# Performance work log

Hardware: AMD Instinct MI355X
Metric: run time of the kernel (lower is better)

The kernel has to match this reference:

```python
import jax, jax.numpy as jnp
import numpy as np

N_NODES = 50000
N_EDGES = 800000
F_IN = 64
CHANNELS = 64
ATTN_SLOPE = 0.2   # GATConv internal LeakyReLU on attention logits
OUT_SLOPE = 0.3    # wrapper's LeakyReLU(alpha=0.3)


def setup_inputs() -> dict:
    key = jax.random.key(0)
    ks = jax.random.split(key, 7)
    x = jax.random.normal(ks[0], (N_NODES, F_IN), dtype=jnp.float32)
    edge_src = jax.random.randint(ks[1], (N_EDGES,), 0, N_NODES, dtype=jnp.int64)
    edge_dst = jax.random.randint(ks[2], (N_EDGES,), 0, N_NODES, dtype=jnp.int64)
    # Learned parameters (single attention head)
    W = jax.random.normal(ks[3], (F_IN, CHANNELS), dtype=jnp.float32) / np.sqrt(F_IN)
    a_src = jax.random.normal(ks[4], (CHANNELS,), dtype=jnp.float32) / np.sqrt(CHANNELS)
    a_dst = jax.random.normal(ks[5], (CHANNELS,), dtype=jnp.float32) / np.sqrt(CHANNELS)
    b = jnp.zeros((CHANNELS,), dtype=jnp.float32)
    return {"x": x, "W": W, "a_src": a_src, "a_dst": a_dst, "b": b,
            "edge_src": edge_src, "edge_dst": edge_dst}


def reference(x, W, a_src, a_dst, b, edge_src, edge_dst):
    N = x.shape[0]
    h = x @ W                                  # [N, C] transformed features
    s_src = h @ a_src                          # [N] per-node source score
    s_dst = h @ a_dst                          # [N] per-node dest score
    # Per-edge attention logits, LeakyReLU(0.2) as in GAT
    e = jax.nn.leaky_relu(s_src[edge_src] + s_dst[edge_dst], ATTN_SLOPE)  # [E]
    # Numerically stable softmax over each destination's neighborhood
    m = jax.ops.segment_max(e, edge_dst, num_segments=N)                  # [N]
    ex = jnp.exp(e - m[edge_dst])                                         # [E]
    denom = jax.ops.segment_sum(ex, edge_dst, num_segments=N)             # [N]
    alpha = ex / jnp.maximum(denom[edge_dst], 1e-9)                       # [E]
    # Scatter-aggregate weighted neighbor features
    out = jax.ops.segment_sum(alpha[:, None] * h[edge_src], edge_dst,
                              num_segments=N) + b                         # [N, C]
    return jax.nn.leaky_relu(out, OUT_SLOPE)
```

## Files before the change

kernel.cpp:

```cpp
#include <hip/hip_runtime.h>
#include <hip/hip_fp16.h>

#define N_NODES 50000
#define N_EDGES 800000
#define CH 64
#define FT_NODES 32
#define FT_BLKS ((N_NODES + FT_NODES - 1) / FT_NODES)
#define NB 782
#define NCHK 784
#define ECHUNK ((N_EDGES + NCHK - 1) / NCHK)
#define LCAP 2048

static constexpr size_t alignup16(size_t x) { return (x + 15) & ~(size_t)15; }
static const size_t OFF_H      = 0;
static const size_t OFF_SSRC   = alignup16(OFF_H      + (size_t)N_NODES*CH*2);
static const size_t OFF_SDST   = alignup16(OFF_SSRC   + (size_t)N_NODES*4);
static const size_t OFF_HIST   = alignup16(OFF_SDST   + (size_t)N_NODES*4);
static const size_t OFF_BTOT   = alignup16(OFF_HIST   + (size_t)NCHK*NB*4);
static const size_t OFF_CB     = alignup16(OFF_BTOT   + (size_t)NB*4);
static const size_t OFF_ROWPTR = alignup16(OFF_CB     + (size_t)(NB+1)*4);
static const size_t OFF_BUCK   = alignup16(OFF_ROWPTR + (size_t)(N_NODES+4)*4);
static const size_t OFF_SPERM  = alignup16(OFF_BUCK   + (size_t)N_EDGES*4);

__global__ __launch_bounds__(256) void k_feat(
        const float* __restrict__ x, const float* __restrict__ W,
        const float* __restrict__ a_src, const float* __restrict__ a_dst,
        const int* __restrict__ edst,
        __half* __restrict__ h, float* __restrict__ ssrc, float* __restrict__ sdst,
        unsigned int* __restrict__ hist) {
    __shared__ float Ws[64 * 64];
    __shared__ float xs[FT_NODES][68];
    __shared__ unsigned int lh[NB];
    const int tid = threadIdx.x;
    const bool do_hist = (blockIdx.x < NCHK);
    if (do_hist)
        for (int j = tid; j < NB; j += 256) lh[j] = 0u;
#pragma unroll
    for (int i = 0; i < 16; ++i) Ws[tid + i * 256] = W[tid + i * 256];
    const int n0 = blockIdx.x * FT_NODES;
    const int nvalid = min(FT_NODES, N_NODES - n0);
    const float4* x4 = (const float4*)(x + (size_t)n0 * CH);
    for (int i = tid; i < nvalid * 16; i += 256) {
        const int n = i >> 4, q = i & 15;
        *(float4*)&xs[n][q * 4] = x4[i];
    }
    __syncthreads();
    if (do_hist) {
        const int st = blockIdx.x * ECHUNK;
        const int en = min(st + ECHUNK, N_EDGES);
        for (int i = st + tid; i < en; i += 256)
            atomicAdd(&lh[((unsigned int)edst[i]) >> 6], 1u);
    }
    const int nl = tid >> 3;
    const int g = tid & 7;
    const int c0 = g * 8;
    const int node = n0 + nl;
    if (nl < nvalid) {
        float acc[8] = {0.f, 0.f, 0.f, 0.f, 0.f, 0.f, 0.f, 0.f};
#pragma unroll
        for (int k = 0; k < 64; ++k) {
            const float xv = xs[nl][k];
            const float4 w0 = *(const float4*)&Ws[k * 64 + c0];
            const float4 w1 = *(const float4*)&Ws[k * 64 + c0 + 4];
            acc[0] = fmaf(xv, w0.x, acc[0]);
            acc[1] = fmaf(xv, w0.y, acc[1]);
            acc[2] = fmaf(xv, w0.z, acc[2]);
            acc[3] = fmaf(xv, w0.w, acc[3]);
            acc[4] = fmaf(xv, w1.x, acc[4]);
            acc[5] = fmaf(xv, w1.y, acc[5]);
            acc[6] = fmaf(xv, w1.z, acc[6]);
            acc[7] = fmaf(xv, w1.w, acc[7]);
        }
        __half2 hv[4];
#pragma unroll
        for (int i = 0; i < 4; ++i) hv[i] = __floats2half2_rn(acc[2 * i], acc[2 * i + 1]);
        *(float4*)(h + (size_t)node * CH + c0) = *(float4*)hv;
        float ps = 0.f, pd = 0.f;
#pragma unroll
        for (int i = 0; i < 8; ++i) {
            ps = fmaf(acc[i], a_src[c0 + i], ps);
            pd = fmaf(acc[i], a_dst[c0 + i], pd);
        }
#pragma unroll
        for (int off = 4; off; off >>= 1) {
            ps += __shfl_xor(ps, off);
            pd += __shfl_xor(pd, off);
        }
        if (g == 0) { ssrc[node] = ps; sdst[node] = pd; }
    }
    if (do_hist) {
        __syncthreads();
        for (int j = tid; j < NB; j += 256)
            hist[(size_t)blockIdx.x * NB + j] = lh[j];
    }
}

__global__ __launch_bounds__(256) void k_bintot(
        const unsigned int* __restrict__ hist, unsigned int* __restrict__ bintot) {
    __shared__ unsigned int red[256];
    const int t = threadIdx.x, b = blockIdx.x;
    unsigned int v = 0u;
    for (int c = t; c < NCHK; c += 256) v += hist[(size_t)c * NB + b];
    red[t] = v;
    __syncthreads();
#pragma unroll
    for (int off = 128; off; off >>= 1) {
        if (t < off) red[t] += red[t + off];
        __syncthreads();
    }
    if (t == 0) bintot[b] = red[0];
}

__global__ __launch_bounds__(256) void k_rewrite(
        const unsigned int* __restrict__ bintot, unsigned int* __restrict__ hist,
        unsigned int* __restrict__ cb) {
    __shared__ unsigned int lcol[NCHK];
    __shared__ unsigned int red[256];
    __shared__ unsigned int sc[256];
    const int t = threadIdx.x, b = blockIdx.x;
    unsigned int v = 0u;
    for (int j = t; j < b; j += 256) v += bintot[j];
    red[t] = v;
    for (int c = t; c < NCHK; c += 256) lcol[c] = hist[(size_t)c * NB + b];
    __syncthreads();
#pragma unroll
    for (int off = 128; off; off >>= 1) {
        if (t < off) red[t] += red[t + off];
        __syncthreads();
    }
    const unsigned int cbb = red[0];
    if (t == 0) { cb[b] = cbb; if (b == NB - 1) cb[NB] = N_EDGES; }
    unsigned int part = 0u;
    const int c0 = 4 * t;
    if (t < 196) {
#pragma unroll
        for (int q = 0; q < 4; ++q) part += lcol[c0 + q];
    }
    sc[t] = part;
    __syncthreads();
#pragma unroll
    for (int off = 1; off < 256; off <<= 1) {
        unsigned int u = (t >= off) ? sc[t - off] : 0u;
        __syncthreads();
        sc[t] += u;
        __syncthreads();
    }
    if (t < 196) {
        unsigned int run = cbb + sc[t] - part;
#pragma unroll
        for (int q = 0; q < 4; ++q) {
            const unsigned int tmp = lcol[c0 + q];
            lcol[c0 + q] = run;
            run += tmp;
        }
    }
    __syncthreads();
    for (int c = t; c < NCHK; c += 256) hist[(size_t)c * NB + b] = lcol[c];
}

__global__ __launch_bounds__(256) void k_scatter(
        const int* __restrict__ esrc, const int* __restrict__ edst,
        const unsigned int* __restrict__ hist, unsigned int* __restrict__ buck) {
    __shared__ unsigned int wp[NB];
    const int t = threadIdx.x, blk = blockIdx.x;
    for (int j = t; j < NB; j += 256) wp[j] = hist[(size_t)blk * NB + j];
    __syncthreads();
    const int st = blk * ECHUNK;
    const int en = min(st + ECHUNK, N_EDGES);
    for (int i = st + t; i < en; i += 256) {
        const unsigned int d = (unsigned int)edst[i];
        const unsigned int pos = atomicAdd(&wp[d >> 6], 1u);
        buck[pos] = (d << 16) | (unsigned int)esrc[i];
    }
}

__global__ __launch_bounds__(256) void k_csr(
        const unsigned int* __restrict__ buck, const unsigned int* __restrict__ cb,
        int* __restrict__ row_ptr, unsigned short* __restrict__ src_perm) {
    __shared__ unsigned int cnt[64];
    __shared__ unsigned int wp[64];
    __shared__ unsigned short lsrc[LCAP];
    const int t = threadIdx.x, blk = blockIdx.x;
    const int start = (int)cb[blk];
    const int end = (int)cb[blk + 1];
    const int m = end - start;
    if (t < 64) cnt[t] = 0u;
    __syncthreads();
    for (int i = start + t; i < end; i += 256)
        atomicAdd(&cnt[(buck[i] >> 16) & 63u], 1u);
    __syncthreads();
    if (t < 64) {
        const unsigned int own = cnt[t];
        unsigned int incl = own;
#pragma unroll
        for (int d = 1; d < 64; d <<= 1) {
            const unsigned int v = __shfl_up(incl, d);
            if (t >= d) incl += v;
        }
        const unsigned int excl = incl - own;
        wp[t] = excl;
        const int node = blk * 64 + t;
        if (node <= N_NODES) row_ptr[node] = start + (int)excl;
    }
    __syncthreads();
    if (m <= LCAP) {
        for (int i = start + t; i < end; i += 256) {
            const unsigned int rec = buck[i];
            const unsigned int pos = atomicAdd(&wp[(rec >> 16) & 63u], 1u);
            lsrc[pos] = (unsigned short)(rec & 0xFFFFu);
        }
        __syncthreads();
        for (int p = t; p < m; p += 256)
            src_perm[start + p] = lsrc[p];
    } else {
        for (int i = start + t; i < end; i += 256) {
            const unsigned int rec = buck[i];
            const unsigned int pos = atomicAdd(&wp[(rec >> 16) & 63u], 1u);
            src_perm[start + (int)pos] = (unsigned short)(rec & 0xFFFFu);
        }
    }
}

__global__ __launch_bounds__(256) void k_node_agg(
        const unsigned short* __restrict__ src_perm, const int* __restrict__ row_ptr,
        const float* __restrict__ ssrc, const float* __restrict__ sdst,
        const __half* __restrict__ h, const float* __restrict__ b,
        float* __restrict__ out) {
    const int tid = threadIdx.x;
    const int lane = tid & 63;
    const int node = blockIdx.x * 4 + (tid >> 6);
    const int row = row_ptr[node];
    const int deg = row_ptr[node + 1] - row;
    const float sd = sdst[node];
    float acc = 0.f;
    float wsum = 0.f;
    for (int base = 0; base < deg; base += 64) {
        const int j = base + lane;
        int s = 0;
        float w = 0.f;
        if (j < deg) {
            s = (int)src_perm[row + j];
            float e = ssrc[s] + sd;
            e = (e > 0.f) ? e : 0.2f * e;
            w = __expf(e);
        }
        wsum += w;
        const int cnt = min(64, deg - base);
        int j2 = 0;
        for (; j2 + 8 <= cnt; j2 += 8) {
            float a[8]; int si[8]; float hv[8];
#pragma unroll
            for (int q = 0; q < 8; ++q) { a[q] = __shfl(w, j2 + q); si[q] = __shfl(s, j2 + q); }
#pragma unroll
            for (int q = 0; q < 8; ++q) hv[q] = __half2float(h[(size_t)si[q] * CH + lane]);
#pragma unroll
            for (int q = 0; q < 8; ++q) acc = fmaf(a[q], hv[q], acc);
        }
        for (; j2 + 4 <= cnt; j2 += 4) {
            float a[4]; int si[4]; float hv[4];
#pragma unroll
            for (int q = 0; q < 4; ++q) { a[q] = __shfl(w, j2 + q); si[q] = __shfl(s, j2 + q); }
#pragma unroll
            for (int q = 0; q < 4; ++q) hv[q] = __half2float(h[(size_t)si[q] * CH + lane]);
#pragma unroll
            for (int q = 0; q < 4; ++q) acc = fmaf(a[q], hv[q], acc);
        }
        for (; j2 < cnt; ++j2) {
            const float a = __shfl(w, j2);
            const int ss = __shfl(s, j2);
            acc = fmaf(a, __half2float(h[(size_t)ss * CH + lane]), acc);
        }
    }
#pragma unroll
    for (int off = 32; off; off >>= 1) wsum += __shfl_xor(wsum, off);
    acc /= fmaxf(wsum, 1e-9f);
    const float v = acc + b[lane];
    out[(size_t)node * CH + lane] = (v > 0.f) ? v : 0.3f * v;
}

extern "C" void kernel_launch(void* const* d_in, const int* in_sizes, int n_in,
                              void* d_out, int out_size, void* d_ws, size_t ws_size,
                              hipStream_t stream) {
    const float* x     = (const float*)d_in[0];
    const float* W     = (const float*)d_in[1];
    const float* a_src = (const float*)d_in[2];
    const float* a_dst = (const float*)d_in[3];
    const float* b     = (const float*)d_in[4];
    const int* esrc    = (const int*)d_in[5];
    const int* edst    = (const int*)d_in[6];
    float* out = (float*)d_out;

    char* ws = (char*)d_ws;
    __half* h                = (__half*)(ws + OFF_H);
    float* ssrc              = (float*)(ws + OFF_SSRC);
    float* sdst              = (float*)(ws + OFF_SDST);
    unsigned int* hist       = (unsigned int*)(ws + OFF_HIST);
    unsigned int* bintot     = (unsigned int*)(ws + OFF_BTOT);
    unsigned int* cb         = (unsigned int*)(ws + OFF_CB);
    int* row_ptr             = (int*)(ws + OFF_ROWPTR);
    unsigned int* buck       = (unsigned int*)(ws + OFF_BUCK);
    unsigned short* src_perm = (unsigned short*)(ws + OFF_SPERM);

    k_feat<<<FT_BLKS, 256, 0, stream>>>(x, W, a_src, a_dst, edst, h, ssrc, sdst, hist);
    k_bintot<<<NB, 256, 0, stream>>>(hist, bintot);
    k_rewrite<<<NB, 256, 0, stream>>>(bintot, hist, cb);
    k_scatter<<<NCHK, 256, 0, stream>>>(esrc, edst, hist, buck);
    k_csr<<<NB, 256, 0, stream>>>(buck, cb, row_ptr, src_perm);
    k_node_agg<<<N_NODES / 4, 256, 0, stream>>>(src_perm, row_ptr, ssrc, sdst, h, b, out);
}
```

Measured before the change: 82.09 us.

## Fuse CSR build with attention aggregation, keeping neighbor lists in shared memory

Result: slower. 93.76 us (+14.2%).

```diff
diff --git a/kernel.cpp b/kernel.cpp
--- a/kernel.cpp
+++ b/kernel.cpp
@@ -9,18 +9,16 @@
 #define NB 782
 #define NCHK 784
 #define ECHUNK ((N_EDGES + NCHK - 1) / NCHK)
-#define LCAP 2048
+#define LCAP 3072
 
 static constexpr size_t alignup16(size_t x) { return (x + 15) & ~(size_t)15; }
-static const size_t OFF_H      = 0;
-static const size_t OFF_SSRC   = alignup16(OFF_H      + (size_t)N_NODES*CH*2);
-static const size_t OFF_SDST   = alignup16(OFF_SSRC   + (size_t)N_NODES*4);
-static const size_t OFF_HIST   = alignup16(OFF_SDST   + (size_t)N_NODES*4);
-static const size_t OFF_BTOT   = alignup16(OFF_HIST   + (size_t)NCHK*NB*4);
-static const size_t OFF_CB     = alignup16(OFF_BTOT   + (size_t)NB*4);
-static const size_t OFF_ROWPTR = alignup16(OFF_CB     + (size_t)(NB+1)*4);
-static const size_t OFF_BUCK   = alignup16(OFF_ROWPTR + (size_t)(N_NODES+4)*4);
-static const size_t OFF_SPERM  = alignup16(OFF_BUCK   + (size_t)N_EDGES*4);
+static const size_t OFF_H    = 0;
+static const size_t OFF_SSRC = alignup16(OFF_H    + (size_t)N_NODES*CH*2);
+static const size_t OFF_SDST = alignup16(OFF_SSRC + (size_t)N_NODES*4);
+static const size_t OFF_HIST = alignup16(OFF_SDST + (size_t)N_NODES*4);
+static const size_t OFF_BTOT = alignup16(OFF_HIST + (size_t)NCHK*NB*4);
+static const size_t OFF_CB   = alignup16(OFF_BTOT + (size_t)NB*4);
+static const size_t OFF_BUCK = alignup16(OFF_CB   + (size_t)(NB+1)*4);
 
 __global__ __launch_bounds__(256) void k_feat(
         const float* __restrict__ x, const float* __restrict__ W,
@@ -174,108 +172,144 @@
     }
 }
 
-__global__ __launch_bounds__(256) void k_csr(
+__global__ __launch_bounds__(512) void k_csr_agg(
         const unsigned int* __restrict__ buck, const unsigned int* __restrict__ cb,
-        int* __restrict__ row_ptr, unsigned short* __restrict__ src_perm) {
+        const float* __restrict__ ssrc, const float* __restrict__ sdst,
+        const __half* __restrict__ h, const float* __restrict__ bias,
+        float* __restrict__ out) {
+    __shared__ unsigned short lsrc[LCAP];
     __shared__ unsigned int cnt[64];
+    __shared__ unsigned int nb[64];
     __shared__ unsigned int wp[64];
-    __shared__ unsigned short lsrc[LCAP];
+    __shared__ float sdL[64];
     const int t = threadIdx.x, blk = blockIdx.x;
     const int start = (int)cb[blk];
     const int end = (int)cb[blk + 1];
     const int m = end - start;
-    if (t < 64) cnt[t] = 0u;
-    __syncthreads();
-    for (int i = start + t; i < end; i += 256)
-        atomicAdd(&cnt[(buck[i] >> 16) & 63u], 1u);
-    __syncthreads();
     if (t < 64) {
-        const unsigned int own = cnt[t];
-        unsigned int incl = own;
-#pragma unroll
-        for (int d = 1; d < 64; d <<= 1) {
-            const unsigned int v = __shfl_up(incl, d);
-            if (t >= d) incl += v;
-        }
-        const unsigned int excl = incl - own;
-        wp[t] = excl;
+        cnt[t] = 0u;
         const int node = blk * 64 + t;
-        if (node <= N_NODES) row_ptr[node] = start + (int)excl;
-    }
-    __syncthreads();
-    if (m <= LCAP) {
-        for (int i = start + t; i < end; i += 256) {
+        sdL[t] = (node < N_NODES) ? sdst[node] : 0.f;
+    }
+    __syncthreads();
+    const bool fits = (m <= LCAP);
+    if (fits) {
+        for (int i = start + t; i < end; i += 512)
+            atomicAdd(&cnt[(buck[i] >> 16) & 63u], 1u);
+        __syncthreads();
+        if (t < 64) {
+            const unsigned int own = cnt[t];
+            unsigned int incl = own;
+#pragma unroll
+            for (int d = 1; d < 64; d <<= 1) {
+                const unsigned int v = __shfl_up(incl, d);
+                if (t >= d) incl += v;
+            }
+            nb[t] = incl - own;
+            wp[t] = incl - own;
+        }
+        __syncthreads();
+        for (int i = start + t; i < end; i += 512) {
             const unsigned int rec = buck[i];
             const unsigned int pos = atomicAdd(&wp[(rec >> 16) & 63u], 1u);
             lsrc[pos] = (unsigned short)(rec & 0xFFFFu);
         }
         __syncthreads();
-        for (int p = t; p < m; p += 256)
-            src_perm[start + p] = lsrc[p];
-    } else {
-        for (int i = start + t; i < end; i += 256) {
-            const unsigned int rec = buck[i];
-            const unsigned int pos = atomicAdd(&wp[(rec >> 16) & 63u], 1u);
-            src_perm[start + (int)pos] = (unsigned short)(rec & 0xFFFFu);
-        }
-    }
-}
-
-__global__ __launch_bounds__(256) void k_node_agg(
-        const unsigned short* __restrict__ src_perm, const int* __restrict__ row_ptr,
-        const float* __restrict__ ssrc, const float* __restrict__ sdst,
-        const __half* __restrict__ h, const float* __restrict__ b,
-        float* __restrict__ out) {
-    const int tid = threadIdx.x;
-    const int lane = tid & 63;
-    const int node = blockIdx.x * 4 + (tid >> 6);
-    const int row = row_ptr[node];
-    const int deg = row_ptr[node + 1] - row;
-    const float sd = sdst[node];
-    float acc = 0.f;
-    float wsum = 0.f;
-    for (int base = 0; base < deg; base += 64) {
-        const int j = base + lane;
-        int s = 0;
-        float w = 0.f;
-        if (j < deg) {
-            s = (int)src_perm[row + j];
-            float e = ssrc[s] + sd;
-            e = (e > 0.f) ? e : 0.2f * e;
-            w = __expf(e);
-        }
-        wsum += w;
-        const int cnt = min(64, deg - base);
-        int j2 = 0;
-        for (; j2 + 8 <= cnt; j2 += 8) {
-            float a[8]; int si[8]; float hv[8];
-#pragma unroll
-            for (int q = 0; q < 8; ++q) { a[q] = __shfl(w, j2 + q); si[q] = __shfl(s, j2 + q); }
-#pragma unroll
-            for (int q = 0; q < 8; ++q) hv[q] = __half2float(h[(size_t)si[q] * CH + lane]);
-#pragma unroll
-            for (int q = 0; q < 8; ++q) acc = fmaf(a[q], hv[q], acc);
-        }
-        for (; j2 + 4 <= cnt; j2 += 4) {
-            float a[4]; int si[4]; float hv[4];
-#pragma unroll
-            for (int q = 0; q < 4; ++q) { a[q] = __shfl(w, j2 + q); si[q] = __shfl(s, j2 + q); }
-#pragma unroll
-            for (int q = 0; q < 4; ++q) hv[q] = __half2float(h[(size_t)si[q] * CH + lane]);
-#pragma unroll
-            for (int q = 0; q < 4; ++q) acc = fmaf(a[q], hv[q], acc);
-        }
-        for (; j2 < cnt; ++j2) {
-            const float a = __shfl(w, j2);
-            const int ss = __shfl(s, j2);
-            acc = fmaf(a, __half2float(h[(size_t)ss * CH + lane]), acc);
-        }
-    }
-#pragma unroll
-    for (int off = 32; off; off >>= 1) wsum += __shfl_xor(wsum, off);
-    acc /= fmaxf(wsum, 1e-9f);
-    const float v = acc + b[lane];
-    out[(size_t)node * CH + lane] = (v > 0.f) ? v : 0.3f * v;
+    }
+    const int wid = t >> 6;
+    const int lane = t & 63;
+    const int slot = lane >> 5;
+    const int c2 = lane & 31;
+    for (int local = wid; local < 64; local += 8) {
+        const int node = blk * 64 + local;
+        if (node >= N_NODES) continue;
+        const float sd = sdL[local];
+        float2 acc = make_float2(0.f, 0.f);
+        float wsum = 0.f;
+        if (fits) {
+            const int base = (int)nb[local];
+            const int deg = (int)cnt[local];
+            for (int tb = 0; tb < deg; tb += 64) {
+                const int cnt_t = min(64, deg - tb);
+                int s = 0;
+                float w = 0.f;
+                if (lane < cnt_t) {
+                    s = (int)lsrc[base + tb + lane];
+                    float e = ssrc[s] + sd;
+                    e = (e > 0.f) ? e : 0.2f * e;
+                    w = __expf(e);
+                }
+                wsum += w;
+                int j2 = 0;
+                for (; j2 + 8 <= cnt_t; j2 += 8) {
+                    float a[4]; int si[4]; __half2 hv[4];
+#pragma unroll
+                    for (int q = 0; q < 4; ++q) {
+                        const int e2 = j2 + 2 * q + slot;
+                        a[q] = __shfl(w, e2);
+                        si[q] = __shfl(s, e2);
+                    }
+#pragma unroll
+                    for (int q = 0; q < 4; ++q)
+                        hv[q] = *(const __half2*)&h[(size_t)si[q] * CH + 2 * c2];
+#pragma unroll
+                    for (int q = 0; q < 4; ++q) {
+                        const float2 f2 = __half22float2(hv[q]);
+                        acc.x = fmaf(a[q], f2.x, acc.x);
+                        acc.y = fmaf(a[q], f2.y, acc.y);
+                    }
+                }
+                for (; j2 < cnt_t; j2 += 2) {
+                    const int e2 = j2 + slot;
+                    const float a = __shfl(w, e2);
+                    const int si = __shfl(s, e2);
+                    const __half2 hv = *(const __half2*)&h[(size_t)si * CH + 2 * c2];
+                    const float2 f2 = __half22float2(hv);
+                    acc.x = fmaf(a, f2.x, acc.x);
+                    acc.y = fmaf(a, f2.y, acc.y);
+                }
+            }
+        } else {
+            for (int i0 = 0; i0 < m; i0 += 64) {
+                int s = 0;
+                float w = 0.f;
+                if (i0 + lane < m) {
+                    const unsigned int rec = buck[start + i0 + lane];
+                    if ((int)(rec >> 16) == node) {
+                        s = (int)(rec & 0xFFFFu);
+                        float e = ssrc[s] + sd;
+                        e = (e > 0.f) ? e : 0.2f * e;
+                        w = __expf(e);
+                    }
+                }
+                wsum += w;
+                for (int j2 = 0; j2 < 64; j2 += 2) {
+                    const int e2 = j2 + slot;
+                    const float a = __shfl(w, e2);
+                    const int si = __shfl(s, e2);
+                    if (a != 0.f) {
+                        const __half2 hv = *(const __half2*)&h[(size_t)si * CH + 2 * c2];
+                        const float2 f2 = __half22float2(hv);
+                        acc.x = fmaf(a, f2.x, acc.x);
+                        acc.y = fmaf(a, f2.y, acc.y);
+                    }
+                }
+            }
+        }
+        acc.x += __shfl_xor(acc.x, 32);
+        acc.y += __shfl_xor(acc.y, 32);
+#pragma unroll
+        for (int off = 32; off; off >>= 1) wsum += __shfl_xor(wsum, off);
+        if (lane < 32) {
+            const float inv = 1.f / fmaxf(wsum, 1e-9f);
+            const float2 bb = *(const float2*)&bias[2 * c2];
+            float vx = acc.x * inv + bb.x;
+            float vy = acc.y * inv + bb.y;
+            vx = (vx > 0.f) ? vx : 0.3f * vx;
+            vy = (vy > 0.f) ? vy : 0.3f * vy;
+            *(float2*)&out[(size_t)node * CH + 2 * c2] = make_float2(vx, vy);
+        }
+    }
 }
 
 extern "C" void kernel_launch(void* const* d_in, const int* in_sizes, int n_in,
@@ -291,20 +325,17 @@
     float* out = (float*)d_out;
 
     char* ws = (char*)d_ws;
-    __half* h                = (__half*)(ws + OFF_H);
-    float* ssrc              = (float*)(ws + OFF_SSRC);
-    float* sdst              = (float*)(ws + OFF_SDST);
-    unsigned int* hist       = (unsigned int*)(ws + OFF_HIST);
-    unsigned int* bintot     = (unsigned int*)(ws + OFF_BTOT);
-    unsigned int* cb         = (unsigned int*)(ws + OFF_CB);
-    int* row_ptr             = (int*)(ws + OFF_ROWPTR);
-    unsigned int* buck       = (unsigned int*)(ws + OFF_BUCK);
-    unsigned short* src_perm = (unsigned short*)(ws + OFF_SPERM);
+    __half* h          = (__half*)(ws + OFF_H);
+    float* ssrc        = (float*)(ws + OFF_SSRC);
+    float* sdst        = (float*)(ws + OFF_SDST);
+    unsigned int* hist = (unsigned int*)(ws + OFF_HIST);
+    unsigned int* bintot = (unsigned int*)(ws + OFF_BTOT);
+    unsigned int* cb   = (unsigned int*)(ws + OFF_CB);
+    unsigned int* buck = (unsigned int*)(ws + OFF_BUCK);
 
     k_feat<<<FT_BLKS, 256, 0, stream>>>(x, W, a_src, a_dst, edst, h, ssrc, sdst, hist);
     k_bintot<<<NB, 256, 0, stream>>>(hist, bintot);
     k_rewrite<<<NB, 256, 0, stream>>>(bintot, hist, cb);
     k_scatter<<<NCHK, 256, 0, stream>>>(esrc, edst, hist, buck);
-    k_csr<<<NB, 256, 0, stream>>>(buck, cb, row_ptr, src_perm);
-    k_node_agg<<<N_NODES / 4, 256, 0, stream>>>(src_perm, row_ptr, ssrc, sdst, h, b, out);
-}
+    k_csr_agg<<<NB, 512, 0, stream>>>(buck, cb, ssrc, sdst, h, b, out);
+}
```

## Process four edges per wavefront step with 8-byte vectorized feature gathers

Applied to the files above, without the earlier changes.

Result: faster. 77.83 us (-5.2%).

```diff
diff --git a/kernel.cpp b/kernel.cpp
--- a/kernel.cpp
+++ b/kernel.cpp
@@ -232,7 +232,9 @@
     const int row = row_ptr[node];
     const int deg = row_ptr[node + 1] - row;
     const float sd = sdst[node];
-    float acc = 0.f;
+    const int slot = lane >> 4;
+    const int c4 = lane & 15;
+    float4 acc = make_float4(0.f, 0.f, 0.f, 0.f);
     float wsum = 0.f;
     for (int base = 0; base < deg; base += 64) {
         const int j = base + lane;
@@ -245,37 +247,50 @@
             w = __expf(e);
         }
         wsum += w;
-        const int cnt = min(64, deg - base);
-        int j2 = 0;
-        for (; j2 + 8 <= cnt; j2 += 8) {
-            float a[8]; int si[8]; float hv[8];
-#pragma unroll
-            for (int q = 0; q < 8; ++q) { a[q] = __shfl(w, j2 + q); si[q] = __shfl(s, j2 + q); }
-#pragma unroll
-            for (int q = 0; q < 8; ++q) hv[q] = __half2float(h[(size_t)si[q] * CH + lane]);
-#pragma unroll
-            for (int q = 0; q < 8; ++q) acc = fmaf(a[q], hv[q], acc);
-        }
-        for (; j2 + 4 <= cnt; j2 += 4) {
-            float a[4]; int si[4]; float hv[4];
-#pragma unroll
-            for (int q = 0; q < 4; ++q) { a[q] = __shfl(w, j2 + q); si[q] = __shfl(s, j2 + q); }
-#pragma unroll
-            for (int q = 0; q < 4; ++q) hv[q] = __half2float(h[(size_t)si[q] * CH + lane]);
-#pragma unroll
-            for (int q = 0; q < 4; ++q) acc = fmaf(a[q], hv[q], acc);
-        }
-        for (; j2 < cnt; ++j2) {
-            const float a = __shfl(w, j2);
-            const int ss = __shfl(s, j2);
-            acc = fmaf(a, __half2float(h[(size_t)ss * CH + lane]), acc);
-        }
-    }
+        const int cnt_t = min(64, deg - base);
+        for (int j2 = 0; j2 < cnt_t; j2 += 16) {
+            float a[4]; int si[4]; float2 raw[4];
+#pragma unroll
+            for (int q = 0; q < 4; ++q) {
+                const int e = j2 + 4 * q + slot;
+                a[q] = __shfl(w, e);
+                si[q] = __shfl(s, e);
+            }
+#pragma unroll
+            for (int q = 0; q < 4; ++q)
+                raw[q] = *(const float2*)&h[(size_t)si[q] * CH + 4 * c4];
+#pragma unroll
+            for (int q = 0; q < 4; ++q) {
+                union { float2 f2; __half2 h2[2]; } u;
+                u.f2 = raw[q];
+                const float2 lo = __half22float2(u.h2[0]);
+                const float2 hi = __half22float2(u.h2[1]);
+                acc.x = fmaf(a[q], lo.x, acc.x);
+                acc.y = fmaf(a[q], lo.y, acc.y);
+                acc.z = fmaf(a[q], hi.x, acc.z);
+                acc.w = fmaf(a[q], hi.y, acc.w);
+            }
+        }
+    }
+    acc.x += __shfl_xor(acc.x, 16); acc.x += __shfl_xor(acc.x, 32);
+    acc.y += __shfl_xor(acc.y, 16); acc.y += __shfl_xor(acc.y, 32);
+    acc.z += __shfl_xor(acc.z, 16); acc.z += __shfl_xor(acc.z, 32);
+    acc.w += __shfl_xor(acc.w, 16); acc.w += __shfl_xor(acc.w, 32);
 #pragma unroll
     for (int off = 32; off; off >>= 1) wsum += __shfl_xor(wsum, off);
-    acc /= fmaxf(wsum, 1e-9f);
-    const float v = acc + b[lane];
-    out[(size_t)node * CH + lane] = (v > 0.f) ? v : 0.3f * v;
+    if (lane < 16) {
+        const float inv = 1.f / fmaxf(wsum, 1e-9f);
+        const float4 bb = *(const float4*)&b[4 * c4];
+        float vx = acc.x * inv + bb.x;
+        float vy = acc.y * inv + bb.y;
+        float vz = acc.z * inv + bb.z;
+        float vw = acc.w * inv + bb.w;
+        vx = (vx > 0.f) ? vx : 0.3f * vx;
+        vy = (vy > 0.f) ? vy : 0.3f * vy;
+        vz = (vz > 0.f) ? vz : 0.3f * vz;
+        vw = (vw > 0.f) ? vw : 0.3f * vw;
+        *(float4*)&out[(size_t)node * CH + 4 * c4] = make_float4(vx, vy, vz, vw);
+    }
 }
 
 extern "C" void kernel_launch(void* const* d_in, const int* in_sizes, int n_in,
```
